# Kernel optimization log

Measured on AMD Instinct MI355X. Metric: run time of the kernel, lower is better.

Reference implementation:

```python
import jax, jax.numpy as jnp
import numpy as np

DEPTH = 12
N_FEATURES = 512
BATCH = 16384
N_NODES = 2 ** DEPTH - 1   # 4095 internal nodes, concatenated level-by-level
N_LEAVES = 2 ** DEPTH      # 4096


def setup_inputs() -> dict:
    key = jax.random.key(0)
    k_x, k_w, k_b, k_s, k_l = jax.random.split(key, 5)
    x_input = jax.random.normal(k_x, (BATCH, N_FEATURES), dtype=jnp.float32)
    # Per-level Linear(n_features, 2**d) weights concatenated on the output dim:
    # level d occupies rows [2**d - 1, 2**(d+1) - 1).
    bound = 1.0 / np.sqrt(N_FEATURES)  # torch Linear default init scale
    W_all = jax.random.uniform(k_w, (N_NODES, N_FEATURES), dtype=jnp.float32,
                               minval=-bound, maxval=bound)
    b_all = jax.random.uniform(k_b, (N_NODES,), dtype=jnp.float32,
                               minval=-bound, maxval=bound)
    # original uses max(randn, 1) -> positive steepness >= 1
    s_all = jax.random.uniform(k_s, (N_NODES,), dtype=jnp.float32,
                               minval=1.0, maxval=2.0)
    leaves = jax.random.normal(k_l, (N_LEAVES,), dtype=jnp.float32)
    return {"x_input": x_input, "W_all": W_all, "b_all": b_all,
            "s_all": s_all, "leaves": leaves}


def reference(x_input, W_all, b_all, s_all, leaves):
    B = x_input.shape[0]
    # One fused GEMM for all depth levels: [B, 2**depth - 1]
    logits = x_input @ W_all.T + b_all
    p_all = jax.nn.sigmoid(logits * s_all)
    # Recursive path-probability product down the binary tree.
    # out[:, j] at level d is the prob of reaching child j (j = 2*node + side),
    # matching the original dict insertion order (node ascending, left then right).
    out = jnp.ones((B, 1), dtype=p_all.dtype)
    for d in range(DEPTH):
        start = 2 ** d - 1
        p = p_all[:, start:start + 2 ** d]          # [B, 2**d]
        # interleave left (parent*p) and right (parent*(1-p)) children
        out = jnp.stack([out * p, out * (1.0 - p)], axis=-1).reshape(B, 2 ** (d + 1))
    # weighted sum over leaves
    return (jax.nn.sigmoid(leaves) * out).sum(axis=1)   # [B]
```

## Files before the change

kernel.cpp:

```cpp
#include <hip/hip_runtime.h>
#include <hip/hip_bf16.h>

#define M_DIM   16384
#define K_DIM   512
#define NNODES  4095
#define NPERM   4096
#define NTOP    128
#define NWROWS  (NPERM + NTOP)
#define NBOT_BLOCKS (32 * 128)
#define NTOT_BLOCKS (NBOT_BLOCKS + 128)

typedef __bf16   bf16x8 __attribute__((ext_vector_type(8)));
typedef float    floatx4 __attribute__((ext_vector_type(4)));

__device__ __forceinline__ float sigmoidf_(float z) {
    return __builtin_amdgcn_rcpf(1.f + __expf(-z));
}

__device__ __forceinline__ void gld_lds16(const void* g, void* l) {
    __builtin_amdgcn_global_load_lds(
        (const __attribute__((address_space(1))) void*)g,
        (__attribute__((address_space(3))) void*)l, 16, 0, 0);
}

__global__ __launch_bounds__(256) void cvt_all(const float* __restrict__ X,
                                               const float* __restrict__ W,
                                               const float* __restrict__ bias,
                                               const float* __restrict__ scale,
                                               __hip_bfloat16* __restrict__ Xb,
                                               __hip_bfloat16* __restrict__ Wb,
                                               float* __restrict__ bp,
                                               float* __restrict__ sp) {
    const int bid = blockIdx.x;
    if (bid < 4096) {
        const int idx = (bid * 256 + threadIdx.x) * 8;
        float4 f0 = *reinterpret_cast<const float4*>(X + idx);
        float4 f1 = *reinterpret_cast<const float4*>(X + idx + 4);
        __hip_bfloat16 h[8];
        h[0] = __float2bfloat16(f0.x); h[1] = __float2bfloat16(f0.y);
        h[2] = __float2bfloat16(f0.z); h[3] = __float2bfloat16(f0.w);
        h[4] = __float2bfloat16(f1.x); h[5] = __float2bfloat16(f1.y);
        h[6] = __float2bfloat16(f1.z); h[7] = __float2bfloat16(f1.w);
        *reinterpret_cast<int4*>(Xb + idx) = *reinterpret_cast<int4*>(h);
        return;
    }
    const int idx = ((bid - 4096) * 256 + threadIdx.x) * 8;
    const int r = idx >> 9;
    const int k = idx & 511;
    int node;
    if (r < NPERM) {
        const int t = r >> 5, o = r & 31;
        int d, q;
        if (o < 16)       { d = 11; q = o; }
        else if (o < 24)  { d = 10; q = o - 16; }
        else if (o < 28)  { d = 9;  q = o - 24; }
        else if (o < 30)  { d = 8;  q = o - 28; }
        else if (o == 30) { d = 7;  q = 0; }
        else              { d = -1; q = 0; }
        node = (d < 0) ? -1 : ((1 << d) - 1 + (t << (d - 7)) + q);
    } else {
        const int c = r - NPERM;
        node = (c < 127) ? c : -1;
    }
    __hip_bfloat16 h[8];
    if (node >= 0) {
        const float* src = W + (size_t)node * 512 + k;
        float4 f0 = *reinterpret_cast<const float4*>(src);
        float4 f1 = *reinterpret_cast<const float4*>(src + 4);
        h[0] = __float2bfloat16(f0.x); h[1] = __float2bfloat16(f0.y);
        h[2] = __float2bfloat16(f0.z); h[3] = __float2bfloat16(f0.w);
        h[4] = __float2bfloat16(f1.x); h[5] = __float2bfloat16(f1.y);
        h[6] = __float2bfloat16(f1.z); h[7] = __float2bfloat16(f1.w);
    } else {
        #pragma unroll
        for (int i = 0; i < 8; ++i) h[i] = __float2bfloat16(0.f);
    }
    *reinterpret_cast<int4*>(Wb + idx) = *reinterpret_cast<int4*>(h);
    if (k == 0) {
        bp[r] = (node >= 0) ? bias[node]  : 0.f;
        sp[r] = (node >= 0) ? scale[node] : 1.f;
    }
}

#define PT_STRIDE 135
__global__ __launch_bounds__(256) void gemm_fold(
    const __hip_bfloat16* __restrict__ A,
    const __hip_bfloat16* __restrict__ B,
    const float* __restrict__ bp,
    const float* __restrict__ sp,
    const float* __restrict__ leaves,
    float* __restrict__ partial,
    _Float16* __restrict__ ptop)
{
    __shared__ char smem[35072] __attribute__((aligned(16)));
    __hip_bfloat16* lA = (__hip_bfloat16*)smem;
    __hip_bfloat16* lB = lA + 8192;
    _Float16* pt  = (_Float16*)smem;
    float*    slf = (float*)(smem + 34560);

    const int tid  = threadIdx.x;
    const int lane = tid & 63;
    const int wv   = tid >> 6;
    const int bid  = blockIdx.x;
    int tile_m, tile_n;
    if (bid < NBOT_BLOCKS) { tile_m = bid >> 5; tile_n = bid & 31; }
    else                   { tile_m = bid - NBOT_BLOCKS; tile_n = 32; }
    const int m0 = tile_m * 128;
    const int n0 = tile_n * 128;

    if (tile_n < 32 && tid < 128) slf[tid] = sigmoidf_(leaves[n0 + tid]);

    const int wm = (wv >> 1) * 64;
    const int wn = (wv & 1) * 64;
    const int lrow = lane >> 3;
    const int swzb = ((lane & 7) ^ lrow) * 16;
    const int quad = lane >> 4;
    const int l15  = lane & 15;
    const int xr   = l15 & 7;

    const char* gAp[4];
    const char* gBp[4];
    __hip_bfloat16* ldsA[4];
    __hip_bfloat16* ldsB[4];
    #pragma unroll
    for (int i = 0; i < 4; ++i) {
        const int rbase = i * 32 + wv * 8;
        gAp[i] = (const char*)(A + (size_t)(m0 + rbase + lrow) * K_DIM) + swzb;
        gBp[i] = (const char*)(B + (size_t)(n0 + rbase + lrow) * K_DIM) + swzb;
        ldsA[i] = lA + rbase * 64;
        ldsB[i] = lB + rbase * 64;
    }

    floatx4 acc[4][4];
    #pragma unroll
    for (int i = 0; i < 4; ++i)
        #pragma unroll
        for (int j = 0; j < 4; ++j)
            acc[i][j] = (floatx4){0.f, 0.f, 0.f, 0.f};

    #pragma unroll 1
    for (int k0 = 0; k0 < K_DIM; k0 += 64) {
        #pragma unroll
        for (int i = 0; i < 4; ++i) {
            gld_lds16(gAp[i], ldsA[i]);
            gld_lds16(gBp[i], ldsB[i]);
            gAp[i] += 128; gBp[i] += 128;
        }
        __syncthreads();
        #pragma unroll
        for (int kk = 0; kk < 64; kk += 32) {
            const int cb = ((kk >> 3) + quad) ^ xr;
            bf16x8 af[4], bfr[4];
            #pragma unroll
            for (int i = 0; i < 4; ++i)
                af[i] = *reinterpret_cast<const bf16x8*>(
                    &lA[(wm + i * 16 + l15) * 64 + cb * 8]);
            #pragma unroll
            for (int j = 0; j < 4; ++j)
                bfr[j] = *reinterpret_cast<const bf16x8*>(
                    &lB[(wn + j * 16 + l15) * 64 + cb * 8]);
            #pragma unroll
            for (int i = 0; i < 4; ++i)
                #pragma unroll
                for (int j = 0; j < 4; ++j)
                    acc[i][j] = __builtin_amdgcn_mfma_f32_16x16x32_bf16(
                        af[i], bfr[j], acc[i][j], 0, 0, 0);
        }
        __syncthreads();
    }

    float bn[4], sn[4];
    #pragma unroll
    for (int j = 0; j < 4; ++j) {
        const int n = n0 + wn + j * 16 + l15;
        bn[j] = bp[n];
        sn[j] = sp[n];
    }

    if (tile_n == 32) {
        #pragma unroll
        for (int i = 0; i < 4; ++i) {
            #pragma unroll
            for (int r = 0; r < 4; ++r) {
                const int m = m0 + wm + i * 16 + quad * 4 + r;
                #pragma unroll
                for (int j = 0; j < 4; ++j) {
                    const int col = wn + j * 16 + l15;
                    ptop[(size_t)m * 128 + col] =
                        (_Float16)sigmoidf_((acc[i][j][r] + bn[j]) * sn[j]);
                }
            }
        }
        return;
    }

    #pragma unroll
    for (int i = 0; i < 4; ++i) {
        #pragma unroll
        for (int r = 0; r < 4; ++r) {
            const int row = wm + i * 16 + quad * 4 + r;
            #pragma unroll
            for (int j = 0; j < 4; ++j) {
                const int col = wn + j * 16 + l15;
                pt[row * PT_STRIDE + col] =
                    (_Float16)sigmoidf_((acc[i][j][r] + bn[j]) * sn[j]);
            }
        }
    }
    __syncthreads();

    #pragma unroll
    for (int z = 0; z < 2; ++z) {
        const int task = tid + z * 256;
        const int row  = task >> 2;
        const int t    = task & 3;
        const _Float16* pp = pt + row * PT_STRIDE + t * 32;
        const float*    sl = slf + t * 32;
        float v[16];
        #pragma unroll
        for (int q = 0; q < 16; ++q) {
            const float p = (float)pp[q];
            v[q] = p * sl[2 * q] + (1.f - p) * sl[2 * q + 1];
        }
        #pragma unroll
        for (int q = 0; q < 8; ++q) {
            const float p = (float)pp[16 + q];
            v[q] = p * v[2 * q] + (1.f - p) * v[2 * q + 1];
        }
        #pragma unroll
        for (int q = 0; q < 4; ++q) {
            const float p = (float)pp[24 + q];
            v[q] = p * v[2 * q] + (1.f - p) * v[2 * q + 1];
        }
        #pragma unroll
        for (int q = 0; q < 2; ++q) {
            const float p = (float)pp[28 + q];
            v[q] = p * v[2 * q] + (1.f - p) * v[2 * q + 1];
        }
        const float p7 = (float)pp[30];
        partial[(size_t)(m0 + row) * 128 + tile_n * 4 + t] =
            p7 * v[0] + (1.f - p7) * v[1];
    }
}

__global__ __launch_bounds__(256) void final_fold(
    const float* __restrict__ partial,
    const _Float16* __restrict__ ptop,
    float* __restrict__ out)
{
    __shared__ float    pL[64 * 129];
    __shared__ _Float16 pq[64 * 134];

    const int tid = threadIdx.x;
    const int m0  = blockIdx.x * 64;

    #pragma unroll
    for (int it = 0; it < 32; ++it) {
        const int idx = tid + it * 256;
        const int row = idx >> 7;
        const int c   = idx & 127;
        pL[row * 129 + c] = partial[(size_t)(m0 + row) * 128 + c];
        pq[row * 134 + c] = ptop[(size_t)(m0 + row) * 128 + c];
    }
    __syncthreads();

    if (tid < 64) {
        float* v = pL + tid * 129;
        const _Float16* pr = pq + tid * 134;
        #pragma unroll
        for (int d = 6; d >= 1; --d) {
            const int base = (1 << d) - 1;
            const int cnt  = 1 << d;
            for (int q = 0; q < cnt; ++q) {
                const float p = (float)pr[base + q];
                v[q] = p * v[2 * q] + (1.f - p) * v[2 * q + 1];
            }
        }
        const float p0 = (float)pr[0];
        out[m0 + tid] = p0 * v[0] + (1.f - p0) * v[1];
    }
}

__global__ __launch_bounds__(256) void tnn_fallback(
    const float* __restrict__ X, const float* __restrict__ W,
    const float* __restrict__ bias, const float* __restrict__ scale,
    const float* __restrict__ leaves, float* __restrict__ out)
{
    __shared__ float xr[512];
    __shared__ float sl[4096];
    __shared__ float pp[4096];
    __shared__ float v0[2048];
    __shared__ float v1[1024];
    const int tid  = threadIdx.x;
    const int lane = tid & 63;
    const int wv   = tid >> 6;
    const int b    = blockIdx.x;
    for (int i = tid; i < 512;  i += 256) xr[i] = X[(size_t)b * 512 + i];
    for (int i = tid; i < 4096; i += 256) sl[i] = sigmoidf_(leaves[i]);
    __syncthreads();
    for (int n = wv; n < NNODES; n += 4) {
        float sum = 0.f;
        const float* wr = W + (size_t)n * 512;
        for (int k = lane; k < 512; k += 64) sum += xr[k] * wr[k];
        #pragma unroll
        for (int off = 32; off; off >>= 1) sum += __shfl_xor(sum, off);
        if (lane == 0) pp[n] = sigmoidf_((sum + bias[n]) * scale[n]);
    }
    __syncthreads();
    for (int j = tid; j < 2048; j += 256) {
        const float p = pp[2047 + j];
        v0[j] = p * sl[2 * j] + (1.f - p) * sl[2 * j + 1];
    }
    __syncthreads();
    float* src = v0;
    float* dst = v1;
    for (int d = 10; d >= 0; --d) {
        const int width = 1 << d;
        const int start = width - 1;
        for (int j = tid; j < width; j += 256) {
            const float p = pp[start + j];
            dst[j] = p * src[2 * j] + (1.f - p) * src[2 * j + 1];
        }
        __syncthreads();
        float* t = src; src = dst; dst = t;
    }
    if (tid == 0) out[b] = src[0];
}

extern "C" void kernel_launch(void* const* d_in, const int* in_sizes, int n_in,
                              void* d_out, int out_size, void* d_ws, size_t ws_size,
                              hipStream_t stream) {
    const float* X      = (const float*)d_in[0];
    const float* W      = (const float*)d_in[1];
    const float* bias   = (const float*)d_in[2];
    const float* scale  = (const float*)d_in[3];
    const float* leaves = (const float*)d_in[4];
    float* out = (float*)d_out;

    const size_t offX  = 0;
    const size_t offW  = (size_t)M_DIM * K_DIM * 2;
    const size_t offB  = offW + (size_t)NWROWS * K_DIM * 2;
    const size_t offS  = offB + (size_t)NWROWS * 4;
    const size_t offP  = offS + (size_t)NWROWS * 4;
    const size_t offT  = offP + (size_t)M_DIM * 128 * 4;
    const size_t need  = offT + (size_t)M_DIM * 128 * 2;

    if (ws_size >= need) {
        __hip_bfloat16* Xb = (__hip_bfloat16*)((char*)d_ws + offX);
        __hip_bfloat16* Wb = (__hip_bfloat16*)((char*)d_ws + offW);
        float* bp = (float*)((char*)d_ws + offB);
        float* sp = (float*)((char*)d_ws + offS);
        float* partial = (float*)((char*)d_ws + offP);
        _Float16* ptop = (_Float16*)((char*)d_ws + offT);
        cvt_all<<<4096 + 1056, 256, 0, stream>>>(X, W, bias, scale, Xb, Wb, bp, sp);
        gemm_fold<<<NTOT_BLOCKS, 256, 0, stream>>>(
            Xb, Wb, bp, sp, leaves, partial, ptop);
        final_fold<<<M_DIM / 64, 256, 0, stream>>>(partial, ptop, out);
    } else {
        tnn_fallback<<<M_DIM, 256, 0, stream>>>(X, W, bias, scale, leaves, out);
    }
}
```

Baseline: 216.6 us.

## Double-buffer LDS tiles in GEMM K-loop to overlap loads with MFMA

Splits shared memory into two A/B tile buffers and prefetches the next K-slice via global_load_lds while computing on the current one. This removes one barrier per iteration and lets global loads overlap MFMA work. In exchange, LDS per block roughly doubles, which reduces how many blocks can be resident per CU and so reduces latency hiding across blocks.

```diff
diff --git a/kernel.cpp b/kernel.cpp
--- a/kernel.cpp
+++ b/kernel.cpp
@@ -83,6 +83,7 @@
 }
 
 #define PT_STRIDE 135
+#define BUFB 32768
 __global__ __launch_bounds__(256) void gemm_fold(
     const __hip_bfloat16* __restrict__ A,
     const __hip_bfloat16* __restrict__ B,
@@ -92,11 +93,9 @@
     float* __restrict__ partial,
     _Float16* __restrict__ ptop)
 {
-    __shared__ char smem[35072] __attribute__((aligned(16)));
-    __hip_bfloat16* lA = (__hip_bfloat16*)smem;
-    __hip_bfloat16* lB = lA + 8192;
+    __shared__ char smem[66560] __attribute__((aligned(16)));
     _Float16* pt  = (_Float16*)smem;
-    float*    slf = (float*)(smem + 34560);
+    float*    slf = (float*)(smem + 66048);
 
     const int tid  = threadIdx.x;
     const int lane = tid & 63;
@@ -120,15 +119,15 @@
 
     const char* gAp[4];
     const char* gBp[4];
-    __hip_bfloat16* ldsA[4];
-    __hip_bfloat16* ldsB[4];
+    char* sA[4];
+    char* sB[4];
     #pragma unroll
     for (int i = 0; i < 4; ++i) {
         const int rbase = i * 32 + wv * 8;
         gAp[i] = (const char*)(A + (size_t)(m0 + rbase + lrow) * K_DIM) + swzb;
         gBp[i] = (const char*)(B + (size_t)(n0 + rbase + lrow) * K_DIM) + swzb;
-        ldsA[i] = lA + rbase * 64;
-        ldsB[i] = lB + rbase * 64;
+        sA[i] = smem + rbase * 128;
+        sB[i] = smem + 16384 + rbase * 128;
     }
 
     floatx4 acc[4][4];
@@ -138,15 +137,28 @@
         for (int j = 0; j < 4; ++j)
             acc[i][j] = (floatx4){0.f, 0.f, 0.f, 0.f};
 
+    #pragma unroll
+    for (int i = 0; i < 4; ++i) {
+        gld_lds16(gAp[i], sA[i]);
+        gld_lds16(gBp[i], sB[i]);
+        gAp[i] += 128; gBp[i] += 128;
+    }
+
     #pragma unroll 1
-    for (int k0 = 0; k0 < K_DIM; k0 += 64) {
-        #pragma unroll
-        for (int i = 0; i < 4; ++i) {
-            gld_lds16(gAp[i], ldsA[i]);
-            gld_lds16(gBp[i], ldsB[i]);
-            gAp[i] += 128; gBp[i] += 128;
-        }
+    for (int k0 = 0; k0 < 8; ++k0) {
         __syncthreads();
+        if (k0 < 7) {
+            const int boff = ((k0 + 1) & 1) * BUFB;
+            #pragma unroll
+            for (int i = 0; i < 4; ++i) {
+                gld_lds16(gAp[i], sA[i] + boff);
+                gld_lds16(gBp[i], sB[i] + boff);
+                gAp[i] += 128; gBp[i] += 128;
+            }
+        }
+        const __hip_bfloat16* cA =
+            (const __hip_bfloat16*)(smem + (k0 & 1) * BUFB);
+        const __hip_bfloat16* cB = cA + 8192;
         #pragma unroll
         for (int kk = 0; kk < 64; kk += 32) {
             const int cb = ((kk >> 3) + quad) ^ xr;
@@ -154,11 +166,11 @@
             #pragma unroll
             for (int i = 0; i < 4; ++i)
                 af[i] = *reinterpret_cast<const bf16x8*>(
-                    &lA[(wm + i * 16 + l15) * 64 + cb * 8]);
+                    &cA[(wm + i * 16 + l15) * 64 + cb * 8]);
             #pragma unroll
             for (int j = 0; j < 4; ++j)
                 bfr[j] = *reinterpret_cast<const bf16x8*>(
-                    &lB[(wn + j * 16 + l15) * 64 + cb * 8]);
+                    &cB[(wn + j * 16 + l15) * 64 + cb * 8]);
             #pragma unroll
             for (int i = 0; i < 4; ++i)
                 #pragma unroll
@@ -166,8 +178,8 @@
                     acc[i][j] = __builtin_amdgcn_mfma_f32_16x16x32_bf16(
                         af[i], bfr[j], acc[i][j], 0, 0, 0);
         }
-        __syncthreads();
-    }
+    }
+    __syncthreads();
 
     float bn[4], sn[4];
     #pragma unroll
```

New measurement: 196.8 us, median of 3. 9.2% less time.
